# Performance work log

Measured on AMD Instinct MI355X. Metric: run time of the kernel, lower is better.

The kernel has to match this reference:

```python
import jax, jax.numpy as jnp
import numpy as np

V, B, C, H, W, D, G = 5, 1, 32, 384, 384, 4, 8


def _rot(a, b, c):
    ca, sa = np.cos(a), np.sin(a)
    cb, sb = np.cos(b), np.sin(b)
    cc, sc = np.cos(c), np.sin(c)
    Rx = np.array([[1, 0, 0], [0, ca, -sa], [0, sa, ca]])
    Ry = np.array([[cb, 0, sb], [0, 1, 0], [-sb, 0, cb]])
    Rz = np.array([[cc, -sc, 0], [sc, cc, 0], [0, 0, 1]])
    return (Rz @ Ry @ Rx).astype(np.float32)


def setup_inputs():
    key = jax.random.key(0)
    ks = jax.random.split(key, 8)
    features = jax.random.normal(ks[0], (V, B, C, H, W), jnp.float32)
    current_depths = jax.random.uniform(ks[1], (B, D, H, W), jnp.float32, 425.0, 935.0)
    rng = np.random.RandomState(0)
    Ks = np.zeros((B, V, 3, 3), np.float32)
    Es = np.zeros((B, V, 3, 4), np.float32)
    for b in range(B):
        for v in range(V):
            f = 0.8 * W * (1.0 + 0.01 * rng.randn())
            Ks[b, v] = np.array([[f, 0, W / 2.0], [0, f, H / 2.0], [0, 0, 1.0]], np.float32)
            if v == 0:
                Rm = np.eye(3, dtype=np.float32)
                t = np.zeros(3, np.float32)
            else:
                Rm = _rot(*(0.02 * rng.randn(3)))
                t = np.array([25.0 * v, 5.0 * rng.randn(), 5.0 * rng.randn()], np.float32)
            Es[b, v, :, :3] = Rm
            Es[b, v, :, 3] = t
    w0 = 0.3 * jax.random.normal(ks[2], (16, G), jnp.float32)
    b0 = jnp.zeros((16,), jnp.float32)
    w1 = 0.3 * jax.random.normal(ks[3], (8, 16), jnp.float32)
    b1 = jnp.zeros((8,), jnp.float32)
    w2 = 0.3 * jax.random.normal(ks[4], (1, 8), jnp.float32)
    b2 = jnp.zeros((1,), jnp.float32)
    return {"features": features, "current_depths": current_depths,
            "cam_intrinsic": jnp.asarray(Ks), "cam_extrinsic": jnp.asarray(Es),
            "w0": w0, "b0": b0, "w1": w1, "b1": b1, "w2": w2, "b2": b2}


def _bilinear_sample(feat, px, py):
    # feat [B,C,H,W]; px,py [B,N] pixel coords (align_corners=True), zero padding
    Bn, Cn, Hn, Wn = feat.shape
    ff = feat.reshape(Bn, Cn, Hn * Wn)
    x0 = jnp.floor(px)
    y0 = jnp.floor(py)
    wx1 = px - x0
    wx0 = 1.0 - wx1
    wy1 = py - y0
    wy0 = 1.0 - wy1

    def gather(xi, yi, w):
        valid = (xi >= 0) & (xi <= Wn - 1) & (yi >= 0) & (yi <= Hn - 1)
        xc = jnp.clip(xi, 0, Wn - 1).astype(jnp.int32)
        yc = jnp.clip(yi, 0, Hn - 1).astype(jnp.int32)
        idx = yc * Wn + xc  # [B,N]
        v = jnp.take_along_axis(ff, idx[:, None, :], axis=2)  # [B,C,N]
        return v * (w * valid)[:, None, :]

    return (gather(x0, y0, wx0 * wy0) + gather(x0 + 1.0, y0, wx1 * wy0)
            + gather(x0, y0 + 1.0, wx0 * wy1) + gather(x0 + 1.0, y0 + 1.0, wx1 * wy1))


def _pixelwise_net(sim, w0, b0, w1, b1, w2, b2):
    # PixelwiseNet: 1x1x1 Conv3d G->16->8->1 (BN folded to identity, eval stats), sigmoid, max over depth
    x = jax.nn.relu(jnp.einsum('og,bgdhw->bodhw', w0, sim) + b0[None, :, None, None, None])
    x = jax.nn.relu(jnp.einsum('oc,bcdhw->bodhw', w1, x) + b1[None, :, None, None, None])
    x = jnp.einsum('oc,bcdhw->bodhw', w2, x) + b2[None, :, None, None, None]
    return jnp.max(jax.nn.sigmoid(x), axis=2)  # [B,1,H,W]


def reference(features, current_depths, cam_intrinsic, cam_extrinsic, w0, b0, w1, b1, w2, b2):
    ref_feat = features[0]                                   # [B,C,H,W]
    ref_g = ref_feat.reshape(B, G, C // G, H, W)
    # pixel grid with half-pixel centers, homogeneous [3, H*W]
    xs = jnp.arange(W, dtype=jnp.float32) + 0.5
    ys = jnp.arange(H, dtype=jnp.float32) + 0.5
    gx, gy = jnp.meshgrid(xs, ys)                            # [H,W]
    grid = jnp.stack([gx.ravel(), gy.ravel(), jnp.ones(H * W, jnp.float32)], 0)
    K_ref_inv = jnp.linalg.inv(cam_intrinsic[:, 0])          # [B,3,3]
    R = cam_extrinsic[:, :, :3, :3]                          # [B,V,3,3]
    t = cam_extrinsic[:, :, :3, 3:4]                         # [B,V,3,1]
    R_ref_inv = jnp.linalg.inv(R[:, 0])                      # [B,3,3]
    uv = jnp.einsum('bij,jn->bin', K_ref_inv, grid)          # [B,3,HW]
    cam_pts = uv[:, None] * current_depths.reshape(B, D, 1, H * W)   # [B,D,3,HW]
    world = jnp.einsum('bij,bdjn->bdin', R_ref_inv, cam_pts - t[:, 0:1])
    world = world.transpose(0, 2, 1, 3).reshape(B, 3, D * H * W)     # [B,3,N], N=D*H*W
    sim_sum = 0.0
    w_sum = 0.0
    for s in range(1, V):
        cp = jnp.einsum('bij,bjn->bin', R[:, s], world) + t[:, s]    # [B,3,N]
        uvd = jnp.einsum('bij,bjn->bin', cam_intrinsic[:, s], cp)
        z = uvd[:, 2] + 1e-9
        px = uvd[:, 0] / z
        py = uvd[:, 1] / z
        warped = _bilinear_sample(features[s], px, py)               # [B,C,N]
        warped = warped.reshape(B, G, C // G, D, H, W)
        sim = jnp.mean(warped * ref_g[:, :, :, None], axis=2)        # [B,G,D,H,W]
        vw = _pixelwise_net(sim, w0, b0, w1, b1, w2, b2)             # [B,1,H,W]
        sim_sum = sim_sum + sim * vw[:, :, None]
        w_sum = w_sum + vw[:, :, None]
    return sim_sum / w_sum
```

## Files before the change

kernel.cpp:

```cpp
#include <hip/hip_runtime.h>
#include <math.h>

#define Vn 5
#define Cn 32
#define Hn 384
#define Wn 384
#define Dn 4
#define Gn 8
#define HWn (Hn*Wn)

typedef _Float16 h2 __attribute__((ext_vector_type(2)));

__device__ __forceinline__ float fdot2h(h2 a, h2 b, float c){
#if __has_builtin(__builtin_amdgcn_fdot2)
    return __builtin_amdgcn_fdot2(a, b, c, false);
#else
    return (float)a.x*(float)b.x + (float)a.y*(float)b.y + c;
#endif
}

__device__ __forceinline__ void inv3(const float* m, float* o){
    float a=m[0],b=m[1],c=m[2],d=m[3],e=m[4],f=m[5],g=m[6],h=m[7],i=m[8];
    float A =  e*i - f*h;
    float B = -(d*i - f*g);
    float C =  d*h - e*g;
    float det = a*A + b*B + c*C;
    float r = 1.f/det;
    o[0] = A*r;            o[1] = -(b*i - c*h)*r;  o[2] =  (b*f - c*e)*r;
    o[3] = B*r;            o[4] =  (a*i - c*g)*r;  o[5] = -(a*f - c*d)*r;
    o[6] = C*r;            o[7] = -(a*h - b*g)*r;  o[8] =  (a*e - b*d)*r;
}
__device__ __forceinline__ void mm3(const float* a, const float* b, float* o){
    #pragma unroll
    for (int r=0;r<3;r++)
        #pragma unroll
        for (int c=0;c<3;c++)
            o[r*3+c] = a[r*3+0]*b[0*3+c] + a[r*3+1]*b[1*3+c] + a[r*3+2]*b[2*3+c];
}
__device__ __forceinline__ void mv3(const float* a, const float* v, float* o){
    #pragma unroll
    for (int r=0;r<3;r++)
        o[r] = a[r*3+0]*v[0] + a[r*3+1]*v[1] + a[r*3+2]*v[2];
}

__device__ __forceinline__ unsigned int packh2(float a, float b){
    h2 h;
    h.x = (_Float16)a;
    h.y = (_Float16)b;
    return __builtin_bit_cast(unsigned int, h);
}

__global__ __launch_bounds__(256)
void transpose_kernel(const float* __restrict__ feat, unsigned short* __restrict__ featT){
    __shared__ float tile[32][257];
    const int s  = blockIdx.y;
    const int p0 = blockIdx.x * 256;
    const int t  = threadIdx.x;
    const float* src = feat + (size_t)(s+1)*Cn*HWn + p0;
    #pragma unroll
    for (int k=0;k<8;k++){
        const int i   = k*256 + t;
        const int px4 = (i & 63) * 4;
        const int ch  = i >> 6;
        const float4 v = *(const float4*)(src + (size_t)ch*HWn + px4);
        tile[ch][px4+0]=v.x; tile[ch][px4+1]=v.y; tile[ch][px4+2]=v.z; tile[ch][px4+3]=v.w;
    }
    __syncthreads();
    uint4* dst = (uint4*)(featT + ((size_t)s*HWn + p0 + t)*Cn);
    #pragma unroll
    for (int q=0;q<4;q++){
        uint4 o;
        o.x = packh2(tile[8*q+0][t], tile[8*q+1][t]);
        o.y = packh2(tile[8*q+2][t], tile[8*q+3][t]);
        o.z = packh2(tile[8*q+4][t], tile[8*q+5][t]);
        o.w = packh2(tile[8*q+6][t], tile[8*q+7][t]);
        dst[q] = o;
    }
}

#define DOTG(uA, uB, g)                                                        \
    {                                                                          \
        const h2 pa = __builtin_bit_cast(h2, (uA));                            \
        const h2 pb = __builtin_bit_cast(h2, (uB));                            \
        const float dt = fdot2h(pa, r2[2*(g)], fdot2h(pb, r2[2*(g)+1], 0.f));  \
        sg[(g)] = fmaf(w, dt, sg[(g)]);                                        \
    }

__device__ __forceinline__ void tap_f16(const unsigned short* __restrict__ vbase,
                                        int xc, int yc, float w,
                                        const h2* r2, float* sg)
{
    if (w != 0.f){
        const uint4* p = (const uint4*)(vbase + ((size_t)yc*Wn + xc)*Cn);
        const uint4 q0 = p[0];
        const uint4 q1 = p[1];
        const uint4 q2 = p[2];
        const uint4 q3 = p[3];
        DOTG(q0.x, q0.y, 0)
        DOTG(q0.z, q0.w, 1)
        DOTG(q1.x, q1.y, 2)
        DOTG(q1.z, q1.w, 3)
        DOTG(q2.x, q2.y, 4)
        DOTG(q2.z, q2.w, 5)
        DOTG(q3.x, q3.y, 6)
        DOTG(q3.z, q3.w, 7)
    }
}

__global__ __launch_bounds__(256, 2)
void gbinet_kernel(const float* __restrict__ feat,
                   const float* __restrict__ depths,
                   const float* __restrict__ Kin,
                   const float* __restrict__ Ein,
                   const float* __restrict__ w0, const float* __restrict__ b0,
                   const float* __restrict__ w1, const float* __restrict__ b1,
                   const float* __restrict__ w2, const float* __restrict__ b2,
                   const unsigned short* __restrict__ featT,
                   float* __restrict__ out)
{
    __shared__ float sW0[128], sW1[128], sB0[16], sB1[8], sW2[8], sB2s[1];
    __shared__ float sM[48];
    __shared__ float sRef[64*33];
    __shared__ float sDep[4*65];
    __shared__ float sOut[64*33];
    const int t = threadIdx.x;
    if (t < 128){ sW0[t] = w0[t]; sW1[t] = w1[t]; }
    if (t < 16) sB0[t] = b0[t];
    if (t < 8){ sB1[t] = b1[t]; sW2[t] = w2[t]; }

    const int blockBase = blockIdx.x * 64;
    {
        const float* srcR = feat + blockBase;
        #pragma unroll
        for (int k=0;k<8;k++){
            const int i  = k*256 + t;
            const int c  = i >> 6;
            const int px = i & 63;
            sRef[px*33 + c] = srcR[(size_t)c*HWn + px];
        }
        const int dp = t >> 6;
        const int px = t & 63;
        sDep[dp*65 + px] = depths[(size_t)dp*HWn + blockBase + px];
    }

    if (t == 0){
        sB2s[0] = b2[0];
        float K0inv[9]; inv3(Kin, K0inv);
        float R0[9], t0[3];
        #pragma unroll
        for (int r=0;r<3;r++){
            #pragma unroll
            for (int c=0;c<3;c++) R0[r*3+c] = Ein[r*4+c];
            t0[r] = Ein[r*4+3];
        }
        float R0inv[9]; inv3(R0, R0inv);
        float M0[9]; mm3(R0inv, K0inv, M0);
        float Rt0[3]; mv3(R0inv, t0, Rt0);
        for (int s=1;s<Vn;s++){
            const float* Ks = Kin + s*9;
            const float* Es = Ein + s*12;
            float Rs[9], ts[3];
            #pragma unroll
            for (int r=0;r<3;r++){
                #pragma unroll
                for (int c=0;c<3;c++) Rs[r*3+c] = Es[r*4+c];
                ts[r] = Es[r*4+3];
            }
            float T1[9]; mm3(Rs, M0, T1);
            float A[9];  mm3(Ks, T1, A);
            float Rr[3]; mv3(Rs, Rt0, Rr);
            float tv[3] = { ts[0]-Rr[0], ts[1]-Rr[1], ts[2]-Rr[2] };
            float cv[3]; mv3(Ks, tv, cv);
            float* dm = &sM[(s-1)*12];
            #pragma unroll
            for (int i=0;i<9;i++) dm[i] = A[i];
            #pragma unroll
            for (int i=0;i<3;i++) dm[9+i] = cv[i];
        }
    }
    __syncthreads();

    const int pixLocal = t >> 2;
    const int s        = t & 3;
    const int pix      = blockBase + pixLocal;
    const float xg = (float)(pix % Wn) + 0.5f;
    const float yg = (float)(pix / Wn) + 0.5f;

    h2 r2[16];
    #pragma unroll
    for (int k=0;k<16;k++){
        r2[k].x = (_Float16)sRef[pixLocal*33 + 2*k];
        r2[k].y = (_Float16)sRef[pixLocal*33 + 2*k+1];
    }
    float dep[Dn];
    #pragma unroll
    for (int d=0;d<Dn;d++) dep[d] = sDep[d*65 + pixLocal];

    const float* M = &sM[s*12];
    const float bx = M[0]*xg + M[1]*yg + M[2];
    const float by = M[3]*xg + M[4]*yg + M[5];
    const float bz = M[6]*xg + M[7]*yg + M[8];
    const float cx = M[9], cy = M[10], cz = M[11];
    const unsigned short* vbase = featT + (size_t)s*HWn*Cn;

    float sim[Gn][Dn];
    #pragma unroll
    for (int d=0;d<Dn;d++){
        const float dd = dep[d];
        const float ux = fmaf(bx, dd, cx);
        const float uy = fmaf(by, dd, cy);
        const float uz = fmaf(bz, dd, cz) + 1e-9f;
        const float rz = 1.f/uz;
        const float px = ux*rz, py = uy*rz;
        const float x0 = floorf(px), y0 = floorf(py);
        const float wx1 = px - x0, wy1 = py - y0;
        const float wx0 = 1.f - wx1, wy0 = 1.f - wy1;
        const bool vx0 = (x0 >= 0.f)     && (x0 <= (float)(Wn-1));
        const bool vx1 = (x0 >= -1.f)    && (x0 <= (float)(Wn-2));
        const bool vy0 = (y0 >= 0.f)     && (y0 <= (float)(Hn-1));
        const bool vy1 = (y0 >= -1.f)    && (y0 <= (float)(Hn-2));
        const float w00 = (vx0&&vy0) ? 0.25f*wx0*wy0 : 0.f;
        const float w10 = (vx1&&vy0) ? 0.25f*wx1*wy0 : 0.f;
        const float w01 = (vx0&&vy1) ? 0.25f*wx0*wy1 : 0.f;
        const float w11 = (vx1&&vy1) ? 0.25f*wx1*wy1 : 0.f;
        const int xi0 = (int)fminf(fmaxf(x0,     0.f), (float)(Wn-1));
        const int xi1 = (int)fminf(fmaxf(x0+1.f, 0.f), (float)(Wn-1));
        const int yi0 = (int)fminf(fmaxf(y0,     0.f), (float)(Hn-1));
        const int yi1 = (int)fminf(fmaxf(y0+1.f, 0.f), (float)(Hn-1));

        float sg[Gn];
        #pragma unroll
        for (int g=0; g<Gn; g++) sg[g] = 0.f;
        tap_f16(vbase, xi0, yi0, w00, r2, sg);
        tap_f16(vbase, xi1, yi0, w10, r2, sg);
        tap_f16(vbase, xi0, yi1, w01, r2, sg);
        tap_f16(vbase, xi1, yi1, w11, r2, sg);
        #pragma unroll
        for (int g=0; g<Gn; g++) sim[g][d] = sg[g];
    }

    float maxlog = -3.0e38f;
    #pragma unroll
    for (int dp=0; dp<2; dp++){
        const int d0 = 2*dp, d1 = 2*dp+1;
        float hx[16], hy[16];
        #pragma unroll
        for (int o=0;o<16;o++){
            float ax = sB0[o], ay = sB0[o];
            #pragma unroll
            for (int g=0; g<Gn; g++){
                const float wv = sW0[o*Gn+g];
                ax = fmaf(wv, sim[g][d0], ax);
                ay = fmaf(wv, sim[g][d1], ay);
            }
            hx[o] = fmaxf(ax, 0.f);
            hy[o] = fmaxf(ay, 0.f);
        }
        float lgx = sB2s[0], lgy = sB2s[0];
        #pragma unroll
        for (int o=0;o<8;o++){
            float ax = sB1[o], ay = sB1[o];
            #pragma unroll
            for (int i=0;i<16;i++){
                const float wv = sW1[o*16+i];
                ax = fmaf(wv, hx[i], ax);
                ay = fmaf(wv, hy[i], ay);
            }
            const float w2v = sW2[o];
            lgx = fmaf(w2v, fmaxf(ax, 0.f), lgx);
            lgy = fmaf(w2v, fmaxf(ay, 0.f), lgy);
        }
        maxlog = fmaxf(maxlog, fmaxf(lgx, lgy));
    }
    const float vw = 1.f/(1.f + __expf(-maxlog));

    float wsum = vw;
    wsum += __shfl_xor(wsum, 1);
    wsum += __shfl_xor(wsum, 2);
    #pragma unroll
    for (int g=0;g<Gn;g++)
        #pragma unroll
        for (int d=0;d<Dn;d++){
            float v = sim[g][d]*vw;
            v += __shfl_xor(v, 1);
            v += __shfl_xor(v, 2);
            sim[g][d] = v;
        }

    if (s == 0){
        const float invw = 1.f/wsum;
        #pragma unroll
        for (int g=0;g<Gn;g++)
            #pragma unroll
            for (int d=0;d<Dn;d++)
                sOut[pixLocal*33 + g*Dn + d] = sim[g][d]*invw;
    }
    __syncthreads();

    float* oBase = out + blockBase;
    #pragma unroll
    for (int k=0;k<8;k++){
        const int e     = k*256 + t;
        const int plane = e >> 6;
        const int pixel = e & 63;
        oBase[(size_t)plane*HWn + pixel] = sOut[pixel*33 + plane];
    }
}

extern "C" void kernel_launch(void* const* d_in, const int* in_sizes, int n_in,
                              void* d_out, int out_size, void* d_ws, size_t ws_size,
                              hipStream_t stream)
{
    (void)in_sizes; (void)n_in; (void)out_size; (void)ws_size;
    const float* feat   = (const float*)d_in[0];
    const float* depths = (const float*)d_in[1];
    const float* K      = (const float*)d_in[2];
    const float* E      = (const float*)d_in[3];
    const float* w0     = (const float*)d_in[4];
    const float* b0     = (const float*)d_in[5];
    const float* w1     = (const float*)d_in[6];
    const float* b1     = (const float*)d_in[7];
    const float* w2     = (const float*)d_in[8];
    const float* b2     = (const float*)d_in[9];
    float* out = (float*)d_out;
    unsigned short* featT = (unsigned short*)d_ws;

    dim3 g(HWn/256, Vn-1);
    transpose_kernel<<<g, 256, 0, stream>>>(feat, featT);
    gbinet_kernel<<<HWn/64, 256, 0, stream>>>(feat, depths, K, E,
                                              w0,b0,w1,b1,w2,b2, featT, out);
}
```

Measured before the change: 242.3 us.

## Split channels across lanes per view and run pixel MLP in packed fp16 dot products

```diff
diff --git a/kernel.cpp b/kernel.cpp
--- a/kernel.cpp
+++ b/kernel.cpp
@@ -18,6 +18,20 @@
     return (float)a.x*(float)b.x + (float)a.y*(float)b.y + c;
 #endif
 }
+__device__ __forceinline__ h2 pkh(float a, float b){
+#if __has_builtin(__builtin_amdgcn_cvt_pkrtz)
+    return __builtin_bit_cast(h2, __builtin_amdgcn_cvt_pkrtz(a, b));
+#else
+    h2 r; r.x = (_Float16)a; r.y = (_Float16)b; return r;
+#endif
+}
+__device__ __forceinline__ unsigned int packh2(float a, float b){
+    h2 h;
+    h.x = (_Float16)a;
+    h.y = (_Float16)b;
+    return __builtin_bit_cast(unsigned int, h);
+}
+__device__ __forceinline__ h2 bch2(unsigned int u){ return __builtin_bit_cast(h2, u); }
 
 __device__ __forceinline__ void inv3(const float* m, float* o){
     float a=m[0],b=m[1],c=m[2],d=m[3],e=m[4],f=m[5],g=m[6],h=m[7],i=m[8];
@@ -43,13 +57,6 @@
         o[r] = a[r*3+0]*v[0] + a[r*3+1]*v[1] + a[r*3+2]*v[2];
 }
 
-__device__ __forceinline__ unsigned int packh2(float a, float b){
-    h2 h;
-    h.x = (_Float16)a;
-    h.y = (_Float16)b;
-    return __builtin_bit_cast(unsigned int, h);
-}
-
 __global__ __launch_bounds__(256)
 void transpose_kernel(const float* __restrict__ feat, unsigned short* __restrict__ featT){
     __shared__ float tile[32][257];
@@ -78,34 +85,52 @@
     }
 }
 
-#define DOTG(uA, uB, g)                                                        \
-    {                                                                          \
-        const h2 pa = __builtin_bit_cast(h2, (uA));                            \
-        const h2 pb = __builtin_bit_cast(h2, (uB));                            \
-        const float dt = fdot2h(pa, r2[2*(g)], fdot2h(pb, r2[2*(g)+1], 0.f));  \
-        sg[(g)] = fmaf(w, dt, sg[(g)]);                                        \
-    }
-
-__device__ __forceinline__ void tap_f16(const unsigned short* __restrict__ vbase,
-                                        int xc, int yc, float w,
-                                        const h2* r2, float* sg)
-{
-    if (w != 0.f){
-        const uint4* p = (const uint4*)(vbase + ((size_t)yc*Wn + xc)*Cn);
-        const uint4 q0 = p[0];
-        const uint4 q1 = p[1];
-        const uint4 q2 = p[2];
-        const uint4 q3 = p[3];
-        DOTG(q0.x, q0.y, 0)
-        DOTG(q0.z, q0.w, 1)
-        DOTG(q1.x, q1.y, 2)
-        DOTG(q1.z, q1.w, 3)
-        DOTG(q2.x, q2.y, 4)
-        DOTG(q2.z, q2.w, 5)
-        DOTG(q3.x, q3.y, 6)
-        DOTG(q3.z, q3.w, 7)
-    }
-}
+#define TAPQ(w_, xi_, yi_, Sv, d_)                                                   \
+    if ((w_) != 0.f){                                                                \
+        const uint4 qd = *(const uint4*)(vb + (size_t)((yi_)*Wn + (xi_))*Cn + q8);   \
+        const float dtA = fdot2h(bch2(qd.x), r2a, fdot2h(bch2(qd.y), r2b, 0.f));     \
+        const float dtB = fdot2h(bch2(qd.z), r2c, fdot2h(bch2(qd.w), r2d, 0.f));     \
+        Sv[2*(d_)+0] = fmaf((w_), dtA, Sv[2*(d_)+0]);                                \
+        Sv[2*(d_)+1] = fmaf((w_), dtB, Sv[2*(d_)+1]);                                \
+    }
+
+#define VIEW_BODY(v_, Sv)                                                            \
+    {                                                                                \
+        const float* M = &sM[(v_)*12];                                               \
+        const float bx = M[0]*xg + M[1]*yg + M[2];                                   \
+        const float by = M[3]*xg + M[4]*yg + M[5];                                   \
+        const float bz = M[6]*xg + M[7]*yg + M[8];                                   \
+        const float cx = M[9], cy = M[10], cz = M[11];                               \
+        const unsigned short* vb = featT + (size_t)(v_)*HWn*Cn;                      \
+        _Pragma("unroll")                                                            \
+        for (int d=0; d<Dn; d++){                                                    \
+            const float dd = dep[d];                                                 \
+            const float ux = fmaf(bx, dd, cx);                                       \
+            const float uy = fmaf(by, dd, cy);                                       \
+            const float uz = fmaf(bz, dd, cz) + 1e-9f;                               \
+            const float rz = 1.f/uz;                                                 \
+            const float px = ux*rz, py = uy*rz;                                      \
+            const float x0 = floorf(px), y0 = floorf(py);                            \
+            const float wx1 = px - x0, wy1 = py - y0;                                \
+            const float wx0 = 1.f - wx1, wy0 = 1.f - wy1;                            \
+            const bool vx0 = (x0 >= 0.f)  && (x0 <= (float)(Wn-1));                  \
+            const bool vx1 = (x0 >= -1.f) && (x0 <= (float)(Wn-2));                  \
+            const bool vy0 = (y0 >= 0.f)  && (y0 <= (float)(Hn-1));                  \
+            const bool vy1 = (y0 >= -1.f) && (y0 <= (float)(Hn-2));                  \
+            const float w00 = (vx0&&vy0) ? 0.25f*wx0*wy0 : 0.f;                      \
+            const float w10 = (vx1&&vy0) ? 0.25f*wx1*wy0 : 0.f;                      \
+            const float w01 = (vx0&&vy1) ? 0.25f*wx0*wy1 : 0.f;                      \
+            const float w11 = (vx1&&vy1) ? 0.25f*wx1*wy1 : 0.f;                      \
+            const int xi0 = (int)fminf(fmaxf(x0,     0.f), (float)(Wn-1));           \
+            const int xi1 = (int)fminf(fmaxf(x0+1.f, 0.f), (float)(Wn-1));           \
+            const int yi0 = (int)fminf(fmaxf(y0,     0.f), (float)(Hn-1));           \
+            const int yi1 = (int)fminf(fmaxf(y0+1.f, 0.f), (float)(Hn-1));           \
+            TAPQ(w00, xi0, yi0, Sv, d)                                               \
+            TAPQ(w10, xi1, yi0, Sv, d)                                               \
+            TAPQ(w01, xi0, yi1, Sv, d)                                               \
+            TAPQ(w11, xi1, yi1, Sv, d)                                               \
+        }                                                                            \
+    }
 
 __global__ __launch_bounds__(256, 2)
 void gbinet_kernel(const float* __restrict__ feat,
@@ -118,15 +143,18 @@
                    const unsigned short* __restrict__ featT,
                    float* __restrict__ out)
 {
-    __shared__ float sW0[128], sW1[128], sB0[16], sB1[8], sW2[8], sB2s[1];
+    __shared__ unsigned int sW0h[64], sW1h[64], sW2h[4];
+    __shared__ float sB0[16], sB1[8], sB2s[1];
     __shared__ float sM[48];
     __shared__ float sRef[64*33];
     __shared__ float sDep[4*65];
     __shared__ float sOut[64*33];
     const int t = threadIdx.x;
-    if (t < 128){ sW0[t] = w0[t]; sW1[t] = w1[t]; }
+    if (t < 64)       sW0h[t]    = packh2(w0[2*t], w0[2*t+1]);
+    else if (t < 128){ const int i = t-64; sW1h[i] = packh2(w1[2*i], w1[2*i+1]); }
+    if (t < 4)  sW2h[t] = packh2(w2[2*t], w2[2*t+1]);
     if (t < 16) sB0[t] = b0[t];
-    if (t < 8){ sB1[t] = b1[t]; sW2[t] = w2[t]; }
+    if (t < 8)  sB1[t] = b1[t];
 
     const int blockBase = blockIdx.x * 64;
     {
@@ -180,120 +208,112 @@
     }
     __syncthreads();
 
-    const int pixLocal = t >> 2;
-    const int s        = t & 3;
-    const int pix      = blockBase + pixLocal;
+    const int pixQ = t >> 2;
+    const int q    = t & 3;
+    const int q8   = q * 8;
+    const int pix  = blockBase + pixQ;
     const float xg = (float)(pix % Wn) + 0.5f;
     const float yg = (float)(pix / Wn) + 0.5f;
 
-    h2 r2[16];
-    #pragma unroll
-    for (int k=0;k<16;k++){
-        r2[k].x = (_Float16)sRef[pixLocal*33 + 2*k];
-        r2[k].y = (_Float16)sRef[pixLocal*33 + 2*k+1];
-    }
+    const h2 r2a = pkh(sRef[pixQ*33 + q8+0], sRef[pixQ*33 + q8+1]);
+    const h2 r2b = pkh(sRef[pixQ*33 + q8+2], sRef[pixQ*33 + q8+3]);
+    const h2 r2c = pkh(sRef[pixQ*33 + q8+4], sRef[pixQ*33 + q8+5]);
+    const h2 r2d = pkh(sRef[pixQ*33 + q8+6], sRef[pixQ*33 + q8+7]);
     float dep[Dn];
     #pragma unroll
-    for (int d=0;d<Dn;d++) dep[d] = sDep[d*65 + pixLocal];
-
-    const float* M = &sM[s*12];
-    const float bx = M[0]*xg + M[1]*yg + M[2];
-    const float by = M[3]*xg + M[4]*yg + M[5];
-    const float bz = M[6]*xg + M[7]*yg + M[8];
-    const float cx = M[9], cy = M[10], cz = M[11];
-    const unsigned short* vbase = featT + (size_t)s*HWn*Cn;
-
-    float sim[Gn][Dn];
-    #pragma unroll
-    for (int d=0;d<Dn;d++){
-        const float dd = dep[d];
-        const float ux = fmaf(bx, dd, cx);
-        const float uy = fmaf(by, dd, cy);
-        const float uz = fmaf(bz, dd, cz) + 1e-9f;
-        const float rz = 1.f/uz;
-        const float px = ux*rz, py = uy*rz;
-        const float x0 = floorf(px), y0 = floorf(py);
-        const float wx1 = px - x0, wy1 = py - y0;
-        const float wx0 = 1.f - wx1, wy0 = 1.f - wy1;
-        const bool vx0 = (x0 >= 0.f)     && (x0 <= (float)(Wn-1));
-        const bool vx1 = (x0 >= -1.f)    && (x0 <= (float)(Wn-2));
-        const bool vy0 = (y0 >= 0.f)     && (y0 <= (float)(Hn-1));
-        const bool vy1 = (y0 >= -1.f)    && (y0 <= (float)(Hn-2));
-        const float w00 = (vx0&&vy0) ? 0.25f*wx0*wy0 : 0.f;
-        const float w10 = (vx1&&vy0) ? 0.25f*wx1*wy0 : 0.f;
-        const float w01 = (vx0&&vy1) ? 0.25f*wx0*wy1 : 0.f;
-        const float w11 = (vx1&&vy1) ? 0.25f*wx1*wy1 : 0.f;
-        const int xi0 = (int)fminf(fmaxf(x0,     0.f), (float)(Wn-1));
-        const int xi1 = (int)fminf(fmaxf(x0+1.f, 0.f), (float)(Wn-1));
-        const int yi0 = (int)fminf(fmaxf(y0,     0.f), (float)(Hn-1));
-        const int yi1 = (int)fminf(fmaxf(y0+1.f, 0.f), (float)(Hn-1));
-
-        float sg[Gn];
-        #pragma unroll
-        for (int g=0; g<Gn; g++) sg[g] = 0.f;
-        tap_f16(vbase, xi0, yi0, w00, r2, sg);
-        tap_f16(vbase, xi1, yi0, w10, r2, sg);
-        tap_f16(vbase, xi0, yi1, w01, r2, sg);
-        tap_f16(vbase, xi1, yi1, w11, r2, sg);
-        #pragma unroll
-        for (int g=0; g<Gn; g++) sim[g][d] = sg[g];
+    for (int d=0;d<Dn;d++) dep[d] = sDep[d*65 + pixQ];
+
+    float S0[8], S1[8], S2[8], S3[8];
+    #pragma unroll
+    for (int k=0;k<8;k++){ S0[k]=0.f; S1[k]=0.f; S2[k]=0.f; S3[k]=0.f; }
+
+    VIEW_BODY(0, S0)
+    VIEW_BODY(1, S1)
+    VIEW_BODY(2, S2)
+    VIEW_BODY(3, S3)
+
+    {
+        const bool c0 = (q & 1);
+        #pragma unroll
+        for (int k=0;k<8;k++){
+            const float p0 = __shfl_xor(S1[k], 1);
+            const float p1 = __shfl_xor(S0[k], 1);
+            const float p2 = __shfl_xor(S3[k], 1);
+            const float p3 = __shfl_xor(S2[k], 1);
+            const float n0 = c0 ? p0 : S0[k];
+            const float n1 = c0 ? S1[k] : p1;
+            const float n2 = c0 ? p2 : S2[k];
+            const float n3 = c0 ? S3[k] : p3;
+            S0[k]=n0; S1[k]=n1; S2[k]=n2; S3[k]=n3;
+        }
+        const bool c1 = (q & 2);
+        #pragma unroll
+        for (int k=0;k<8;k++){
+            const float p0 = __shfl_xor(S2[k], 2);
+            const float p1 = __shfl_xor(S3[k], 2);
+            const float p2 = __shfl_xor(S0[k], 2);
+            const float p3 = __shfl_xor(S1[k], 2);
+            const float n0 = c1 ? p0 : S0[k];
+            const float n1 = c1 ? p1 : S1[k];
+            const float n2 = c1 ? S2[k] : p2;
+            const float n3 = c1 ? S3[k] : p3;
+            S0[k]=n0; S1[k]=n1; S2[k]=n2; S3[k]=n3;
+        }
     }
 
     float maxlog = -3.0e38f;
     #pragma unroll
-    for (int dp=0; dp<2; dp++){
-        const int d0 = 2*dp, d1 = 2*dp+1;
-        float hx[16], hy[16];
+    for (int d=0; d<Dn; d++){
+        const h2 s0 = pkh(S0[2*d], S0[2*d+1]);
+        const h2 s1 = pkh(S1[2*d], S1[2*d+1]);
+        const h2 s2 = pkh(S2[2*d], S2[2*d+1]);
+        const h2 s3 = pkh(S3[2*d], S3[2*d+1]);
+        float h[16];
         #pragma unroll
         for (int o=0;o<16;o++){
-            float ax = sB0[o], ay = sB0[o];
-            #pragma unroll
-            for (int g=0; g<Gn; g++){
-                const float wv = sW0[o*Gn+g];
-                ax = fmaf(wv, sim[g][d0], ax);
-                ay = fmaf(wv, sim[g][d1], ay);
-            }
-            hx[o] = fmaxf(ax, 0.f);
-            hy[o] = fmaxf(ay, 0.f);
-        }
-        float lgx = sB2s[0], lgy = sB2s[0];
+            float a = sB0[o];
+            a = fdot2h(bch2(sW0h[o*4+0]), s0, a);
+            a = fdot2h(bch2(sW0h[o*4+1]), s1, a);
+            a = fdot2h(bch2(sW0h[o*4+2]), s2, a);
+            a = fdot2h(bch2(sW0h[o*4+3]), s3, a);
+            h[o] = fmaxf(a, 0.f);
+        }
+        h2 hp[8];
+        #pragma unroll
+        for (int i=0;i<8;i++) hp[i] = pkh(h[2*i], h[2*i+1]);
+        float g8[8];
         #pragma unroll
         for (int o=0;o<8;o++){
-            float ax = sB1[o], ay = sB1[o];
-            #pragma unroll
-            for (int i=0;i<16;i++){
-                const float wv = sW1[o*16+i];
-                ax = fmaf(wv, hx[i], ax);
-                ay = fmaf(wv, hy[i], ay);
-            }
-            const float w2v = sW2[o];
-            lgx = fmaf(w2v, fmaxf(ax, 0.f), lgx);
-            lgy = fmaf(w2v, fmaxf(ay, 0.f), lgy);
-        }
-        maxlog = fmaxf(maxlog, fmaxf(lgx, lgy));
+            float a = sB1[o];
+            #pragma unroll
+            for (int i=0;i<8;i++) a = fdot2h(bch2(sW1h[o*8+i]), hp[i], a);
+            g8[o] = fmaxf(a, 0.f);
+        }
+        float lg = sB2s[0];
+        #pragma unroll
+        for (int i=0;i<4;i++) lg = fdot2h(bch2(sW2h[i]), pkh(g8[2*i], g8[2*i+1]), lg);
+        maxlog = fmaxf(maxlog, lg);
     }
     const float vw = 1.f/(1.f + __expf(-maxlog));
 
     float wsum = vw;
     wsum += __shfl_xor(wsum, 1);
     wsum += __shfl_xor(wsum, 2);
-    #pragma unroll
-    for (int g=0;g<Gn;g++)
-        #pragma unroll
-        for (int d=0;d<Dn;d++){
-            float v = sim[g][d]*vw;
-            v += __shfl_xor(v, 1);
-            v += __shfl_xor(v, 2);
-            sim[g][d] = v;
-        }
-
-    if (s == 0){
-        const float invw = 1.f/wsum;
-        #pragma unroll
-        for (int g=0;g<Gn;g++)
-            #pragma unroll
-            for (int d=0;d<Dn;d++)
-                sOut[pixLocal*33 + g*Dn + d] = sim[g][d]*invw;
+    const float invw = 1.f/wsum;
+    #pragma unroll
+    for (int k=0;k<8;k++){
+        float v0 = S0[k]*vw, v1 = S1[k]*vw, v2 = S2[k]*vw, v3 = S3[k]*vw;
+        v0 += __shfl_xor(v0, 1); v0 += __shfl_xor(v0, 2);
+        v1 += __shfl_xor(v1, 1); v1 += __shfl_xor(v1, 2);
+        v2 += __shfl_xor(v2, 1); v2 += __shfl_xor(v2, 2);
+        v3 += __shfl_xor(v3, 1); v3 += __shfl_xor(v3, 2);
+        if (q == 0){
+            const int d = k >> 1, j = k & 1;
+            sOut[pixQ*33 + (0+j)*Dn + d] = v0*invw;
+            sOut[pixQ*33 + (2+j)*Dn + d] = v1*invw;
+            sOut[pixQ*33 + (4+j)*Dn + d] = v2*invw;
+            sOut[pixQ*33 + (6+j)*Dn + d] = v3*invw;
+        }
     }
     __syncthreads();
 
```

New measurement: 312.8 us. +29.1%, slower.
